# Optimization experiments

Measured on AMD Instinct MI355X. Metric: run time of the kernel, lower is better.

Reference implementation:

```python
import jax, jax.numpy as jnp
import numpy as np

S, B, V, E, H = 64, 32, 32000, 512, 1024


def gru_cell(x, h, Wih, Whh, bih, bhh):
    # PyTorch GRU cell math. x: [B, in], h: [B, H]
    gi = x @ Wih.T + bih          # [B, 3H]
    gh = h @ Whh.T + bhh          # [B, 3H]
    ir, iz, inn = jnp.split(gi, 3, axis=-1)
    hr, hz, hn = jnp.split(gh, 3, axis=-1)
    r = jax.nn.sigmoid(ir + hr)
    z = jax.nn.sigmoid(iz + hz)
    n = jnp.tanh(inn + r * hn)
    return (1.0 - z) * n + z * h


def run_gru(xs, h0, Wih, Whh, bih, bhh):
    def step(h, x):
        h = gru_cell(x, h, Wih, Whh, bih, bhh)
        return h, h
    _, hs = jax.lax.scan(step, h0, xs)
    return hs  # [S, B, H]


def setup_inputs():
    key = jax.random.key(0)
    ks = jax.random.split(key, 24)
    n = lambda k, shp, s=0.05: (jax.random.normal(k, shp, jnp.float32) * s)
    inp = {
        "input_seq": jax.random.randint(ks[0], (S, B), 0, V),
        "target_seq": jax.random.randint(ks[1], (S, B), 0, V),
        "emb": n(ks[2], (V, E)),
        # bidirectional encoder GRU (forward / backward directions)
        "enc_Wih_f": n(ks[3], (3 * H, E)), "enc_Whh_f": n(ks[4], (3 * H, H)),
        "enc_bih_f": n(ks[5], (3 * H,)),  "enc_bhh_f": n(ks[6], (3 * H,)),
        "enc_Wih_b": n(ks[7], (3 * H, E)), "enc_Whh_b": n(ks[8], (3 * H, H)),
        "enc_bih_b": n(ks[9], (3 * H,)),  "enc_bhh_b": n(ks[10], (3 * H,)),
        "encoder_init": n(ks[11], (2, H), 0.1),
        # decoder GRU: input = token(E) + glimpse(2H) + last_output(E)
        "dec_Wih": n(ks[12], (3 * H, 2 * E + 2 * H)), "dec_Whh": n(ks[13], (3 * H, H)),
        "dec_bih": n(ks[14], (3 * H,)), "dec_bhh": n(ks[15], (3 * H,)),
        "dec_init_h": n(ks[16], (H,), 0.1),
        "dec_init_out": n(ks[17], (E,), 0.1),
        "attn_W1": n(ks[18], (H, 3 * H)),  # Linear(3H -> H, bias=False)
        "attn_W2": n(ks[19], (1, H)),      # Linear(H -> 1, bias=False)
        "out_W": n(ks[20], (V, H)), "out_b": n(ks[21], (V,)),
    }
    return inp


def reference(input_seq, target_seq, emb,
              enc_Wih_f, enc_Whh_f, enc_bih_f, enc_bhh_f,
              enc_Wih_b, enc_Whh_b, enc_bih_b, enc_bhh_b, encoder_init,
              dec_Wih, dec_Whh, dec_bih, dec_bhh, dec_init_h, dec_init_out,
              attn_W1, attn_W2, out_W, out_b):
    x = emb[input_seq]            # [S, B, E]
    tgt = emb[target_seq]         # [S, B, E]
    bsz = x.shape[1]

    # bidirectional encoder
    h0f = jnp.broadcast_to(encoder_init[0], (bsz, H))
    h0b = jnp.broadcast_to(encoder_init[1], (bsz, H))
    fwd = run_gru(x, h0f, enc_Wih_f, enc_Whh_f, enc_bih_f, enc_bhh_f)
    bwd = run_gru(x[::-1], h0b, enc_Wih_b, enc_Whh_b, enc_bih_b, enc_bhh_b)[::-1]
    enc = jnp.concatenate([fwd, bwd], axis=-1)  # [S, B, 2H]

    def step(carry, inp_t):
        h, last_out = carry                      # [B,H], [B,E]
        tok, tg = inp_t                          # [B,E], [B,E]
        hexp = jnp.broadcast_to(h[None], (S, bsz, H))
        a = jnp.concatenate([enc, hexp], axis=-1)            # [S, B, 3H]
        scores = jnp.tanh(a @ attn_W1.T) @ attn_W2.T          # [S, B, 1]
        # NOTE: original uses nn.Softmax(dim=1) on [S,B,1] -> softmax over BATCH dim
        w = jax.nn.softmax(scores, axis=1)
        glimpse = (enc * w).sum(axis=0)                       # [B, 2H]
        dec_in = jnp.concatenate([tok, glimpse, last_out], axis=-1)
        h = gru_cell(dec_in, h, dec_Wih, dec_Whh, dec_bih, dec_bhh)
        probs = jax.nn.softmax(h @ out_W.T + out_b, axis=1)   # [B, V]
        return (h, tg), probs

    h0 = jnp.broadcast_to(dec_init_h, (bsz, H))
    o0 = jnp.broadcast_to(dec_init_out, (bsz, E))
    _, outs = jax.lax.scan(step, (h0, o0), (x, tgt))
    return outs  # [S, B, V]
```

## Files before the change

### kernel.cpp

```cpp
#include <hip/hip_runtime.h>
#include <hip/hip_bf16.h>

#define S_ 64
#define B_ 32
#define V_ 32000
#define E_ 512
#define H_ 1024
#define H3_ 3072

typedef __hip_bfloat16 bf16;
typedef __attribute__((ext_vector_type(8))) short s8v;
typedef __attribute__((ext_vector_type(4))) float f4;
typedef unsigned long long ull;

__device__ __forceinline__ float b2f(bf16 x){ return __bfloat162float(x); }
__device__ __forceinline__ bf16  f2b(float x){ return __float2bfloat16(x); }
__device__ __forceinline__ float bfu2f(unsigned short u){
  union { unsigned u; float f; } c; c.u = ((unsigned)u) << 16; return c.f;
}
#define MFMA16(a,b,c) __builtin_amdgcn_mfma_f32_16x16x32_bf16((a),(b),(c),0,0,0)

__device__ __forceinline__ float fsigmoid(float x){ return 1.f/(1.f + __expf(-x)); }
__device__ __forceinline__ float ftanh(float x){ float e2 = __expf(2.f*x); return 1.f - 2.f/(e2 + 1.f); }

__global__ __launch_bounds__(256) void cast_bf16_k(const float* __restrict__ s, bf16* __restrict__ d, int n8){
  int stride = gridDim.x*256;
  for (int i = blockIdx.x*256 + threadIdx.x; i < n8; i += stride){
    f4 a = *((const f4*)s + (size_t)i*2);
    f4 b = *((const f4*)s + (size_t)i*2 + 1);
    union { s8v v; bf16 h[8]; } o;
    #pragma unroll
    for (int k=0;k<4;k++){ o.h[k]=f2b(a[k]); o.h[4+k]=f2b(b[k]); }
    *((s8v*)d + i) = o.v;
  }
}
__global__ __launch_bounds__(256) void gather_x_k(const float* __restrict__ emb, const int* __restrict__ seq, bf16* __restrict__ d){
  int i = blockIdx.x*256 + threadIdx.x;
  int row = i >> 6, e8 = i & 63;
  const float* src = emb + (size_t)seq[row]*E_;
  f4 a = *((const f4*)src + e8*2);
  f4 b = *((const f4*)src + e8*2 + 1);
  union { s8v v; bf16 h[8]; } o;
  #pragma unroll
  for (int k=0;k<4;k++){ o.h[k]=f2b(a[k]); o.h[4+k]=f2b(b[k]); }
  *((s8v*)d + i) = o.v;
}
__global__ __launch_bounds__(256) void gather_lo_k(const float* __restrict__ emb, const int* __restrict__ tseq, const float* __restrict__ o0, bf16* __restrict__ d){
  int i = blockIdx.x*256 + threadIdx.x;
  int row = i >> 6, e8 = i & 63;
  int t = row >> 5, b = row & 31;
  const float* src = (t == 0) ? o0 : (emb + (size_t)tseq[(t-1)*B_ + b]*E_);
  f4 a = *((const f4*)src + e8*2);
  f4 c = *((const f4*)src + e8*2 + 1);
  union { s8v v; bf16 h[8]; } o;
  #pragma unroll
  for (int k=0;k<4;k++){ o.h[k]=f2b(a[k]); o.h[4+k]=f2b(c[k]); }
  *((s8v*)d + i) = o.v;
}

template<int WB16, int ACC>
__global__ __launch_bounds__(256) void gemm_bt(const bf16* __restrict__ A, int lda,
                                               const bf16* __restrict__ B, int ldb,
                                               const float* __restrict__ bias,
                                               void* __restrict__ Cp, int ldc, int K)
{
  __shared__ bf16 a_sm[128][40];
  __shared__ bf16 b_sm[128][40];
  const int tid = threadIdx.x;
  const int m0 = blockIdx.y*128, n0 = blockIdx.x*128;
  const int w = tid>>6, l = tid&63;
  const int wm = w>>1, wn = w&1;
  f4 acc[4][4];
  #pragma unroll
  for (int i=0;i<4;i++)
    #pragma unroll
    for (int j=0;j<4;j++) acc[i][j] = (f4){0.f,0.f,0.f,0.f};
  const int srow = tid>>1, skc = (tid&1)*16;
  const int ar = l&15, koff = (l>>4)*8;
  for (int k0 = 0; k0 < K; k0 += 32){
    __syncthreads();
    const s8v* pa = (const s8v*)(A + (size_t)(m0+srow)*lda + k0 + skc);
    const s8v* pb = (const s8v*)(B + (size_t)(n0+srow)*ldb + k0 + skc);
    *(s8v*)&a_sm[srow][skc]   = pa[0];
    *(s8v*)&a_sm[srow][skc+8] = pa[1];
    *(s8v*)&b_sm[srow][skc]   = pb[0];
    *(s8v*)&b_sm[srow][skc+8] = pb[1];
    __syncthreads();
    s8v av[4], bv[4];
    #pragma unroll
    for (int i=0;i<4;i++) av[i] = *(const s8v*)&a_sm[wm*64 + i*16 + ar][koff];
    #pragma unroll
    for (int j=0;j<4;j++) bv[j] = *(const s8v*)&b_sm[wn*64 + j*16 + ar][koff];
    #pragma unroll
    for (int i=0;i<4;i++)
      #pragma unroll
      for (int j=0;j<4;j++)
        acc[i][j] = MFMA16(av[i], bv[j], acc[i][j]);
  }
  const int rb = (l>>4)*4;
  #pragma unroll
  for (int i=0;i<4;i++){
    #pragma unroll
    for (int j=0;j<4;j++){
      int col = n0 + wn*64 + j*16 + ar;
      float badd = bias ? bias[col] : 0.f;
      #pragma unroll
      for (int r=0;r<4;r++){
        int row = m0 + wm*64 + i*16 + rb + r;
        size_t idx = (size_t)row*ldc + col;
        float v = acc[i][j][r] + badd;
        if (ACC) v += ((const float*)Cp)[idx];
        if (WB16) ((bf16*)Cp)[idx] = f2b(v);
        else      ((float*)Cp)[idx] = v;
      }
    }
  }
}

__global__ __launch_bounds__(256) void enc_init_k(const float* __restrict__ enc_init,
                                                  bf16* __restrict__ hb0, float* __restrict__ hfE){
  int i = blockIdx.x*256 + threadIdx.x;
  int base = i*8;
  int dir = base>>15, rem = base&32767, col = rem&1023;
  const float* sp = enc_init + dir*H_ + col;
  f4 a = *(const f4*)sp, b = *(const f4*)(sp+4);
  union { s8v v; bf16 h[8]; } o;
  #pragma unroll
  for (int k=0;k<4;k++){ o.h[k]=f2b(a[k]); o.h[4+k]=f2b(b[k]); }
  *(s8v*)(hb0 + dir*32768 + rem) = o.v;
  *(f4*)(hfE + dir*32768 + rem) = a;
  *(f4*)(hfE + dir*32768 + rem + 4) = b;
}
__global__ __launch_bounds__(256) void dec_init_k(const float* __restrict__ dinh,
                                                  bf16* __restrict__ hd0, float* __restrict__ hfD){
  int i = blockIdx.x*256 + threadIdx.x;
  int base = i*8;
  int col = base&1023;
  const float* sp = dinh + col;
  f4 a = *(const f4*)sp, b = *(const f4*)(sp+4);
  union { s8v v; bf16 h[8]; } o;
  #pragma unroll
  for (int k=0;k<4;k++){ o.h[k]=f2b(a[k]); o.h[4+k]=f2b(b[k]); }
  *(s8v*)(hd0 + base) = o.v;
  *(f4*)(hfD + base) = a;
  *(f4*)(hfD + base + 4) = b;
}

__global__ __launch_bounds__(256) void enc_step_k(
  const float* __restrict__ gi_f, const float* __restrict__ gi_b,
  const bf16* __restrict__ whhf, const bf16* __restrict__ whhb,
  const float* __restrict__ bhhf, const float* __restrict__ bhhb,
  const bf16* __restrict__ hrd_base,
  bf16* __restrict__ hwr_base,
  float* __restrict__ hfE,
  bf16* __restrict__ enc_out, int s)
{
  __shared__ bf16 hst[16][1032];
  __shared__ bf16 hsT[16][64];
  const int tid = threadIdx.x, bid = blockIdx.x;
  const int w = tid>>6, l = tid&63;
  const int lr = l&15, koff = (l>>4)*8, rb = (l>>4)*4;
  const int x = bid&7, g3 = bid>>3;
  const int dir = x>>2;
  const int mt = g3>>2;
  const int jtb = (x&3)*16 + (g3&3)*4;
  const int jt = jtb + w;
  const int col = jt*16 + lr;
  const bf16* W    = dir ? whhb : whhf;
  const float* gi  = dir ? gi_b : gi_f;
  const float* bhh = dir ? bhhb : bhhf;
  const float br_ = bhh[col], bz_ = bhh[H_+col], bn_ = bhh[2*H_+col];
  const bf16* pr = W + (size_t)(jt*16 + lr)*H_ + koff;
  const bf16* pz = pr + (size_t)H_*H_;
  const bf16* pn = pz + (size_t)H_*H_;
  {
    const bf16* src = hrd_base + dir*32768 + (size_t)mt*16*H_;
    #pragma unroll
    for (int c = 0; c < 8; ++c){
      int g = c*256 + tid;
      int row = g>>7, off = g&127;
      *(s8v*)&hst[row][off*8] = *(const s8v*)(src + (size_t)row*H_ + off*8);
    }
  }
  __syncthreads();
  f4 accr = (f4){0,0,0,0}, accz = (f4){0,0,0,0}, accn = (f4){0,0,0,0};
  #pragma unroll 4
  for (int k0 = 0; k0 < H_; k0 += 32){
    s8v a = *(const s8v*)&hst[lr][koff + k0];
    accr = MFMA16(a, *(const s8v*)(pr + k0), accr);
    accz = MFMA16(a, *(const s8v*)(pz + k0), accz);
    accn = MFMA16(a, *(const s8v*)(pn + k0), accn);
  }
  const int es = dir ? (63 - s) : s;
  #pragma unroll
  for (int ri = 0; ri < 4; ++ri){
    const int b_ = mt*16 + rb + ri;
    const size_t gr = (size_t)(es*B_ + b_)*H3_;
    float ir = gi[gr + col], iz = gi[gr + H_ + col], inn = gi[gr + 2*H_ + col];
    float rg = fsigmoid(ir + accr[ri] + br_);
    float zg = fsigmoid(iz + accz[ri] + bz_);
    float ng = ftanh(inn + rg*(accn[ri] + bn_));
    float hold = hfE[dir*32768 + b_*H_ + col];
    float hnew = (1.f - zg)*ng + zg*hold;
    hfE[dir*32768 + b_*H_ + col] = hnew;
    hsT[rb+ri][w*16+lr] = f2b(hnew);
  }
  __syncthreads();
  {
    const int row = tid>>4, seg = tid&15;
    ull v = *(ull*)&hsT[row][seg*4];
    *(ull*)(hwr_base + dir*32768 + (size_t)(mt*16+row)*H_ + jtb*16 + seg*4) = v;
    *(ull*)(enc_out + (size_t)(es*B_ + mt*16+row)*2048 + dir*H_ + jtb*16 + seg*4) = v;
  }
}

__global__ __launch_bounds__(256) void dec_k1(
  const bf16* __restrict__ hd,
  const bf16* __restrict__ whhd, const float* __restrict__ bhhd,
  const bf16* __restrict__ w1b,
  float* __restrict__ gh, bf16* __restrict__ hW1b)
{
  __shared__ bf16 hst[16][1032];
  __shared__ float ghT[16][128];
  __shared__ bf16 hwT[16][128];
  const int tid = threadIdx.x, bid = blockIdx.x;
  const int w = tid>>6, l = tid&63;
  const int lr = l&15, koff = (l>>4)*8;
  const bool isP = bid < 16;
  const int hmt = isP ? (bid&1) : ((bid-16)&1);
  {
    const bf16* src = hd + (size_t)hmt*16*H_;
    #pragma unroll
    for (int c = 0; c < 8; ++c){
      int g = c*256 + tid;
      int row = g>>7, off = g&127;
      *(s8v*)&hst[row][off*8] = *(const s8v*)(src + (size_t)row*H_ + off*8);
    }
  }
  __syncthreads();
  if (isP){
    const int x2 = bid>>1;
    const int pjt0 = x2*8 + w*2;
    #pragma unroll
    for (int q = 0; q < 2; ++q){
      const bf16* pb = w1b + (size_t)((pjt0+q)*16 + lr)*H3_ + 2048 + koff;
      f4 acc = (f4){0,0,0,0};
      #pragma unroll 4
      for (int k0 = 0; k0 < H_; k0 += 32)
        acc = MFMA16(*(const s8v*)&hst[lr][koff+k0], *(const s8v*)(pb+k0), acc);
      #pragma unroll
      for (int r = 0; r < 4; ++r)
        hwT[(l>>4)*4+r][(w*2+q)*16 + lr] = f2b(acc[r]);
    }
    __syncthreads();
    #pragma unroll
    for (int i = 0; i < 2; ++i){
      int idx = tid + i*256;
      int row = idx>>5, seg = idx&31;
      *(ull*)(hW1b + (size_t)(hmt*16+row)*H_ + x2*128 + seg*4) = *(ull*)&hwT[row][seg*4];
    }
  } else {
    const int gb = bid - 16;
    const int rest = gb>>1;
    const int x3 = rest/3, gkk = rest%3;
    const int ntb = x3*24 + gkk*8;
    #pragma unroll
    for (int q = 0; q < 2; ++q){
      const int nt = ntb + w*2 + q;
      const bf16* pb = whhd + (size_t)(nt*16 + lr)*H_ + koff;
      const float bv = bhhd[nt*16 + lr];
      f4 acc = (f4){0,0,0,0};
      #pragma unroll 4
      for (int k0 = 0; k0 < H_; k0 += 32)
        acc = MFMA16(*(const s8v*)&hst[lr][koff+k0], *(const s8v*)(pb+k0), acc);
      #pragma unroll
      for (int r = 0; r < 4; ++r)
        ghT[(l>>4)*4+r][(w*2+q)*16 + lr] = acc[r] + bv;
    }
    __syncthreads();
    #pragma unroll
    for (int i = 0; i < 4; ++i){
      int idx = tid + i*256;
      int row = idx>>6, seg = idx&63;
      union{ float f[2]; ull u; } pk;
      pk.f[0] = ghT[row][seg*2]; pk.f[1] = ghT[row][seg*2+1];
      *(ull*)(gh + (size_t)(hmt*16+row)*H3_ + ntb*16 + seg*2) = pk.u;
    }
  }
}

__global__ __launch_bounds__(256) void dec_k2(
  const bf16* __restrict__ encW1b, const bf16* __restrict__ hW1b,
  const float* __restrict__ attnW2, float* __restrict__ wat)
{
  __shared__ float w2st[1024];
  __shared__ float scl[32];
  const int tid = threadIdx.x, s = blockIdx.x;
  w2st[tid] = attnW2[tid];
  w2st[tid+256] = attnW2[tid+256];
  w2st[tid+512] = attnW2[tid+512];
  w2st[tid+768] = attnW2[tid+768];
  __syncthreads();
  const int b = tid>>3, part = tid&7;
  const bf16* hp = hW1b + (size_t)b*H_ + part*128;
  const bf16* ep = encW1b + ((size_t)s*B_ + b)*H_ + part*128;
  const float* wp = w2st + part*128;
  float p = 0.f;
  #pragma unroll 4
  for (int ii = 0; ii < 16; ++ii){
    union { s8v v; unsigned short uu[8]; } hv, ev;
    hv.v = *(const s8v*)(hp + ii*8);
    ev.v = *(const s8v*)(ep + ii*8);
    #pragma unroll
    for (int k = 0; k < 8; ++k){
      float xx = bfu2f(ev.uu[k]) + bfu2f(hv.uu[k]);
      p += wp[ii*8+k]*ftanh(xx);
    }
  }
  p += __shfl_xor(p,1); p += __shfl_xor(p,2); p += __shfl_xor(p,4);
  if (part == 0) scl[b] = p;
  __syncthreads();
  if (tid < 32){
    float v = scl[tid];
    float m = v;
    #pragma unroll
    for (int o = 1; o <= 16; o <<= 1) m = fmaxf(m, __shfl_xor(m, o));
    float e = __expf(v - m);
    float Z = e;
    #pragma unroll
    for (int o = 1; o <= 16; o <<= 1) Z += __shfl_xor(Z, o);
    wat[s*B_ + tid] = e/Z;
  }
}

__global__ __launch_bounds__(256) void dec_k3(
  const float* __restrict__ gi_t,
  const bf16* __restrict__ encWgb, const float* __restrict__ gh,
  const float* __restrict__ wat,
  float* __restrict__ hfD, bf16* __restrict__ hd_w, bf16* __restrict__ hall_t)
{
  __shared__ float watst[64];
  __shared__ float part_[4][3][256];
  __shared__ bf16 hnewst[256];
  const int tid = threadIdx.x, bid = blockIdx.x;
  const int x = bid&7, g3 = bid>>3;
  const int db = 4*x + (g3&3), jq = g3>>2;
  const int jD = jq*256 + tid;
  if (tid < 64) watst[tid] = wat[tid*B_ + db];
  __syncthreads();
  const int lane = tid&63, wv = tid>>6;
  const int j0 = jq*256 + lane*4;
  f4 g0 = (f4){0,0,0,0}, g1 = (f4){0,0,0,0}, g2 = (f4){0,0,0,0};
  #pragma unroll 4
  for (int i = 0; i < 16; ++i){
    const int s2 = wv*16 + i;
    const float wt = watst[s2];
    const bf16* ro = encWgb + ((size_t)s2*B_ + db)*H3_;
    union{ ull u; unsigned short us[4]; } v0, v1, v2;
    v0.u = *(const ull*)(ro + j0);
    v1.u = *(const ull*)(ro + H_ + j0);
    v2.u = *(const ull*)(ro + 2*H_ + j0);
    #pragma unroll
    for (int k = 0; k < 4; ++k){
      g0[k] += wt*bfu2f(v0.us[k]);
      g1[k] += wt*bfu2f(v1.us[k]);
      g2[k] += wt*bfu2f(v2.us[k]);
    }
  }
  *(f4*)&part_[wv][0][lane*4] = g0;
  *(f4*)&part_[wv][1][lane*4] = g1;
  *(f4*)&part_[wv][2][lane*4] = g2;
  __syncthreads();
  float G0 = part_[0][0][tid]+part_[1][0][tid]+part_[2][0][tid]+part_[3][0][tid];
  float G1 = part_[0][1][tid]+part_[1][1][tid]+part_[2][1][tid]+part_[3][1][tid];
  float G2 = part_[0][2][tid]+part_[1][2][tid]+part_[2][2][tid]+part_[3][2][tid];
  const float* gp = gi_t + (size_t)db*H3_ + jD;
  float ir  = gp[0]    + G0;
  float iz  = gp[H_]   + G1;
  float inn = gp[2*H_] + G2;
  float hr_ = gh[(size_t)db*H3_ + jD];
  float hz_ = gh[(size_t)db*H3_ + H_ + jD];
  float hn_ = gh[(size_t)db*H3_ + 2*H_ + jD];
  float rg = fsigmoid(ir + hr_);
  float zg = fsigmoid(iz + hz_);
  float ng = ftanh(inn + rg*hn_);
  float hold = hfD[(size_t)db*H_ + jD];
  float hnew = (1.f - zg)*ng + zg*hold;
  hfD[(size_t)db*H_ + jD] = hnew;
  hnewst[tid] = f2b(hnew);
  __syncthreads();
  if (tid < 64){
    ull v = *(ull*)&hnewst[tid*4];
    *(ull*)(hd_w + (size_t)db*H_ + jq*256 + tid*4) = v;
    *(ull*)(hall_t + (size_t)db*H_ + jq*256 + tid*4) = v;
  }
}

__global__ __launch_bounds__(256) void softmax_rows_k(float* __restrict__ out){
  __shared__ float wm[4], wl[4];
  const int tid = threadIdx.x;
  float* p = out + (size_t)blockIdx.x*V_;
  float m = -1e30f, lsum = 0.f;
  for (int j = tid; j < V_; j += 256){
    float v = p[j];
    float mn = fmaxf(m, v);
    lsum = lsum*__expf(m - mn) + __expf(v - mn);
    m = mn;
  }
  #pragma unroll
  for (int o = 32; o; o >>= 1){
    float mo = __shfl_xor(m, o), lo_ = __shfl_xor(lsum, o);
    float mn = fmaxf(m, mo);
    lsum = lsum*__expf(m - mn) + lo_*__expf(mo - mn);
    m = mn;
  }
  if ((tid&63)==0){ wm[tid>>6] = m; wl[tid>>6] = lsum; }
  __syncthreads();
  float M = fmaxf(fmaxf(wm[0],wm[1]), fmaxf(wm[2],wm[3]));
  float L = wl[0]*__expf(wm[0]-M) + wl[1]*__expf(wm[1]-M)
          + wl[2]*__expf(wm[2]-M) + wl[3]*__expf(wm[3]-M);
  float inv = 1.f/L;
  for (int j = tid; j < V_; j += 256) p[j] = __expf(p[j]-M)*inv;
}

extern "C" void kernel_launch(void* const* d_in, const int* in_sizes, int n_in,
                              void* d_out, int out_size, void* d_ws, size_t ws_size,
                              hipStream_t stream)
{
  (void)in_sizes; (void)n_in; (void)out_size; (void)ws_size;
  const int*   iseq  = (const int*)d_in[0];
  const int*   tseq  = (const int*)d_in[1];
  const float* emb   = (const float*)d_in[2];
  const float* wihf  = (const float*)d_in[3];
  const float* whhf_f= (const float*)d_in[4];
  const float* bihf  = (const float*)d_in[5];
  const float* bhhf  = (const float*)d_in[6];
  const float* wihb  = (const float*)d_in[7];
  const float* whhb_f= (const float*)d_in[8];
  const float* bihb  = (const float*)d_in[9];
  const float* bhhb  = (const float*)d_in[10];
  const float* einit = (const float*)d_in[11];
  const float* wihd  = (const float*)d_in[12];
  const float* whhd_f= (const float*)d_in[13];
  const float* bihd  = (const float*)d_in[14];
  const float* bhhd  = (const float*)d_in[15];
  const float* dinh  = (const float*)d_in[16];
  const float* dino  = (const float*)d_in[17];
  const float* w1    = (const float*)d_in[18];
  const float* w2    = (const float*)d_in[19];
  const float* outw  = (const float*)d_in[20];
  const float* outb  = (const float*)d_in[21];
  float* out = (float*)d_out;

  char* ws = (char*)d_ws;
  size_t off = 0;
  auto alloc = [&](size_t bytes)->char*{ char* p = ws + off; off += (bytes + 255) & ~(size_t)255; return p; };
  bf16* x_b      = (bf16*)alloc((size_t)2048*512*2);
  bf16* lo_b     = (bf16*)alloc((size_t)2048*512*2);
  bf16* wihf_b   = (bf16*)alloc((size_t)3072*512*2);
  bf16* wihb_b   = (bf16*)alloc((size_t)3072*512*2);
  bf16* whhf_b   = (bf16*)alloc((size_t)3072*1024*2);
  bf16* whhb_b   = (bf16*)alloc((size_t)3072*1024*2);
  bf16* wihd_b   = (bf16*)alloc((size_t)3072*3072*2);
  bf16* whhd_b   = (bf16*)alloc((size_t)3072*1024*2);
  bf16* w1_b     = (bf16*)alloc((size_t)1024*3072*2);
  bf16* outw_b   = (bf16*)alloc((size_t)32000*1024*2);
  float* gi_f    = (float*)alloc((size_t)2048*3072*4);
  float* gi_b    = (float*)alloc((size_t)2048*3072*4);
  float* gi_d    = (float*)alloc((size_t)2048*3072*4);
  bf16* enc_b    = (bf16*)alloc((size_t)2048*2048*2);
  bf16* encW1_b  = (bf16*)alloc((size_t)2048*1024*2);
  bf16* encWg_b  = (bf16*)alloc((size_t)2048*3072*2);
  bf16*  henc_b  = (bf16*)alloc((size_t)2*65536*2);
  float* hfE     = (float*)alloc((size_t)2*32768*4);
  bf16*  hdb     = (bf16*)alloc((size_t)2*32768*2);
  float* hfD     = (float*)alloc((size_t)32768*4);
  bf16*  hW1b    = (bf16*)alloc((size_t)32768*2);
  float* ghb     = (float*)alloc((size_t)32*3072*4);
  float* wat     = (float*)alloc((size_t)64*32*4);
  bf16*  hall_b  = (bf16*)alloc((size_t)2048*1024*2);

  auto cgrid = [](int n8){ int g = (n8 + 255)/256; return g > 2048 ? 2048 : g; };
  gather_x_k <<<512, 256, 0, stream>>>(emb, iseq, x_b);
  gather_lo_k<<<512, 256, 0, stream>>>(emb, tseq, dino, lo_b);
  cast_bf16_k<<<cgrid(196608),  256, 0, stream>>>(wihf,   wihf_b, 196608);
  cast_bf16_k<<<cgrid(196608),  256, 0, stream>>>(wihb,   wihb_b, 196608);
  cast_bf16_k<<<cgrid(393216),  256, 0, stream>>>(whhf_f, whhf_b, 393216);
  cast_bf16_k<<<cgrid(393216),  256, 0, stream>>>(whhb_f, whhb_b, 393216);
  cast_bf16_k<<<cgrid(1179648), 256, 0, stream>>>(wihd,   wihd_b, 1179648);
  cast_bf16_k<<<cgrid(393216),  256, 0, stream>>>(whhd_f, whhd_b, 393216);
  cast_bf16_k<<<cgrid(393216),  256, 0, stream>>>(w1,     w1_b,   393216);
  cast_bf16_k<<<cgrid(4096000), 256, 0, stream>>>(outw,   outw_b, 4096000);

  gemm_bt<0,0><<<dim3(24,16), 256, 0, stream>>>(x_b, 512, wihf_b,      512,  bihf,    gi_f, 3072, 512);
  gemm_bt<0,0><<<dim3(24,16), 256, 0, stream>>>(x_b, 512, wihb_b,      512,  bihb,    gi_b, 3072, 512);
  gemm_bt<0,0><<<dim3(24,16), 256, 0, stream>>>(x_b, 512, wihd_b,      3072, bihd,    gi_d, 3072, 512);
  gemm_bt<0,1><<<dim3(24,16), 256, 0, stream>>>(lo_b,512, wihd_b+2560, 3072, nullptr, gi_d, 3072, 512);

  enc_init_k<<<32, 256, 0, stream>>>(einit, henc_b, hfE);
  for (int s = 0; s < 64; ++s){
    const bf16* hrd = henc_b + (size_t)(s&1)*65536;
    bf16*       hwr = henc_b + (size_t)((s+1)&1)*65536;
    enc_step_k<<<64, 256, 0, stream>>>(gi_f, gi_b, whhf_b, whhb_b, bhhf, bhhb,
                                       hrd, hwr, hfE, enc_b, s);
  }

  gemm_bt<1,0><<<dim3(8,16),  256, 0, stream>>>(enc_b, 2048, w1_b,       3072, nullptr, encW1_b, 1024, 2048);
  gemm_bt<1,0><<<dim3(24,16), 256, 0, stream>>>(enc_b, 2048, wihd_b+512, 3072, nullptr, encWg_b, 3072, 2048);

  dec_init_k<<<16, 256, 0, stream>>>(dinh, hdb, hfD);
  for (int t = 0; t < 64; ++t){
    const bf16* hdr = hdb + (size_t)(t&1)*32768;
    bf16*       hdw = hdb + (size_t)((t+1)&1)*32768;
    dec_k1<<<64, 256, 0, stream>>>(hdr, whhd_b, bhhd, w1_b, ghb, hW1b);
    dec_k2<<<64, 256, 0, stream>>>(encW1_b, hW1b, w2, wat);
    dec_k3<<<128, 256, 0, stream>>>(gi_d + (size_t)t*B_*H3_, encWg_b, ghb, wat,
                                    hfD, hdw, hall_b + (size_t)t*B_*H_);
  }

  gemm_bt<0,0><<<dim3(250,16), 256, 0, stream>>>(hall_b, 1024, outw_b, 1024, outb, out, 32000, 1024);
  softmax_rows_k<<<2048, 256, 0, stream>>>(out);
}
```

Before: 3.279 ms.

## Fuse decoder attention score kernel into hidden-projection kernel and batch weight casts

Merges the decoder per-step kernels from three to two. The h·W1 projection and the tanh/W2 attention-score reduction now run in the same blocks of the first kernel, each writing partial scores per quarter of H, and the batch softmax moves into the gate kernel. It also combines the forward and backward encoder input GEMMs into a single 6144-wide GEMM with a concatenated bias, and groups the weight casts into fewer launches. The goal is fewer launches and less serialisation in the 64-step decoder loop. The cost is redundant softmax work in every gate block and an extra partial-score buffer.

```diff
diff --git a/kernel.cpp b/kernel.cpp
--- a/kernel.cpp
+++ b/kernel.cpp
@@ -24,6 +24,36 @@
 __device__ __forceinline__ float ftanh(float x){ float e2 = __expf(2.f*x); return 1.f - 2.f/(e2 + 1.f); }
 
 __global__ __launch_bounds__(256) void cast_bf16_k(const float* __restrict__ s, bf16* __restrict__ d, int n8){
+  int stride = gridDim.x*256;
+  for (int i = blockIdx.x*256 + threadIdx.x; i < n8; i += stride){
+    f4 a = *((const f4*)s + (size_t)i*2);
+    f4 b = *((const f4*)s + (size_t)i*2 + 1);
+    union { s8v v; bf16 h[8]; } o;
+    #pragma unroll
+    for (int k=0;k<4;k++){ o.h[k]=f2b(a[k]); o.h[4+k]=f2b(b[k]); }
+    *((s8v*)d + i) = o.v;
+  }
+}
+__global__ __launch_bounds__(256) void cast2_k(const float* __restrict__ s0, const float* __restrict__ s1,
+                                               bf16* __restrict__ d0, bf16* __restrict__ d1, int n8){
+  const float* s = blockIdx.y ? s1 : s0;
+  bf16* d = blockIdx.y ? d1 : d0;
+  int stride = gridDim.x*256;
+  for (int i = blockIdx.x*256 + threadIdx.x; i < n8; i += stride){
+    f4 a = *((const f4*)s + (size_t)i*2);
+    f4 b = *((const f4*)s + (size_t)i*2 + 1);
+    union { s8v v; bf16 h[8]; } o;
+    #pragma unroll
+    for (int k=0;k<4;k++){ o.h[k]=f2b(a[k]); o.h[4+k]=f2b(b[k]); }
+    *((s8v*)d + i) = o.v;
+  }
+}
+__global__ __launch_bounds__(256) void cast4_k(const float* __restrict__ s0, const float* __restrict__ s1,
+                                               const float* __restrict__ s2, const float* __restrict__ s3,
+                                               bf16* __restrict__ d0, bf16* __restrict__ d1,
+                                               bf16* __restrict__ d2, bf16* __restrict__ d3, int n8){
+  const float* s = (blockIdx.y==0)?s0:(blockIdx.y==1)?s1:(blockIdx.y==2)?s2:s3;
+  bf16* d = (blockIdx.y==0)?d0:(blockIdx.y==1)?d1:(blockIdx.y==2)?d2:d3;
   int stride = gridDim.x*256;
   for (int i = blockIdx.x*256 + threadIdx.x; i < n8; i += stride){
     f4 a = *((const f4*)s + (size_t)i*2);
@@ -118,7 +148,9 @@
 }
 
 __global__ __launch_bounds__(256) void enc_init_k(const float* __restrict__ enc_init,
-                                                  bf16* __restrict__ hb0, float* __restrict__ hfE){
+                                                  const float* __restrict__ bihf, const float* __restrict__ bihb,
+                                                  bf16* __restrict__ hb0, float* __restrict__ hfE,
+                                                  float* __restrict__ bias_fb){
   int i = blockIdx.x*256 + threadIdx.x;
   int base = i*8;
   int dir = base>>15, rem = base&32767, col = rem&1023;
@@ -130,6 +162,7 @@
   *(s8v*)(hb0 + dir*32768 + rem) = o.v;
   *(f4*)(hfE + dir*32768 + rem) = a;
   *(f4*)(hfE + dir*32768 + rem + 4) = b;
+  if (i < 6144) bias_fb[i] = (i < 3072) ? bihf[i] : bihb[i-3072];
 }
 __global__ __launch_bounds__(256) void dec_init_k(const float* __restrict__ dinh,
                                                   bf16* __restrict__ hd0, float* __restrict__ hfD){
@@ -147,13 +180,11 @@
 }
 
 __global__ __launch_bounds__(256) void enc_step_k(
-  const float* __restrict__ gi_f, const float* __restrict__ gi_b,
+  const float* __restrict__ gi_fb,
   const bf16* __restrict__ whhf, const bf16* __restrict__ whhb,
   const float* __restrict__ bhhf, const float* __restrict__ bhhb,
-  const bf16* __restrict__ hrd_base,
-  bf16* __restrict__ hwr_base,
-  float* __restrict__ hfE,
-  bf16* __restrict__ enc_out, int s)
+  const bf16* __restrict__ hrd_base, bf16* __restrict__ hwr_base,
+  float* __restrict__ hfE, bf16* __restrict__ enc_out, int s)
 {
   __shared__ bf16 hst[16][1032];
   __shared__ bf16 hsT[16][64];
@@ -167,7 +198,6 @@
   const int jt = jtb + w;
   const int col = jt*16 + lr;
   const bf16* W    = dir ? whhb : whhf;
-  const float* gi  = dir ? gi_b : gi_f;
   const float* bhh = dir ? bhhb : bhhf;
   const float br_ = bhh[col], bz_ = bhh[H_+col], bn_ = bhh[2*H_+col];
   const bf16* pr = W + (size_t)(jt*16 + lr)*H_ + koff;
@@ -192,11 +222,12 @@
     accn = MFMA16(a, *(const s8v*)(pn + k0), accn);
   }
   const int es = dir ? (63 - s) : s;
+  const int dcol = dir*3072 + col;
   #pragma unroll
   for (int ri = 0; ri < 4; ++ri){
     const int b_ = mt*16 + rb + ri;
-    const size_t gr = (size_t)(es*B_ + b_)*H3_;
-    float ir = gi[gr + col], iz = gi[gr + H_ + col], inn = gi[gr + 2*H_ + col];
+    const size_t gr = (size_t)(es*B_ + b_)*6144;
+    float ir = gi_fb[gr + dcol], iz = gi_fb[gr + 1024 + dcol], inn = gi_fb[gr + 2048 + dcol];
     float rg = fsigmoid(ir + accr[ri] + br_);
     float zg = fsigmoid(iz + accz[ri] + bz_);
     float ng = ftanh(inn + rg*(accn[ri] + bn_));
@@ -214,56 +245,37 @@
   }
 }
 
-__global__ __launch_bounds__(256) void dec_k1(
+__global__ __launch_bounds__(256) void dec_kA(
   const bf16* __restrict__ hd,
   const bf16* __restrict__ whhd, const float* __restrict__ bhhd,
   const bf16* __restrict__ w1b,
-  float* __restrict__ gh, bf16* __restrict__ hW1b)
+  const bf16* __restrict__ encW1b,
+  const float* __restrict__ attnW2,
+  float* __restrict__ gh,
+  float* __restrict__ sc4)
 {
   __shared__ bf16 hst[16][1032];
   __shared__ float ghT[16][128];
-  __shared__ bf16 hwT[16][128];
+  __shared__ bf16 hbst[1024];
+  __shared__ float hw1s[256];
   const int tid = threadIdx.x, bid = blockIdx.x;
   const int w = tid>>6, l = tid&63;
   const int lr = l&15, koff = (l>>4)*8;
-  const bool isP = bid < 16;
-  const int hmt = isP ? (bid&1) : ((bid-16)&1);
-  {
-    const bf16* src = hd + (size_t)hmt*16*H_;
-    #pragma unroll
-    for (int c = 0; c < 8; ++c){
-      int g = c*256 + tid;
-      int row = g>>7, off = g&127;
-      *(s8v*)&hst[row][off*8] = *(const s8v*)(src + (size_t)row*H_ + off*8);
-    }
-  }
-  __syncthreads();
-  if (isP){
-    const int x2 = bid>>1;
-    const int pjt0 = x2*8 + w*2;
-    #pragma unroll
-    for (int q = 0; q < 2; ++q){
-      const bf16* pb = w1b + (size_t)((pjt0+q)*16 + lr)*H3_ + 2048 + koff;
-      f4 acc = (f4){0,0,0,0};
-      #pragma unroll 4
-      for (int k0 = 0; k0 < H_; k0 += 32)
-        acc = MFMA16(*(const s8v*)&hst[lr][koff+k0], *(const s8v*)(pb+k0), acc);
-      #pragma unroll
-      for (int r = 0; r < 4; ++r)
-        hwT[(l>>4)*4+r][(w*2+q)*16 + lr] = f2b(acc[r]);
-    }
-    __syncthreads();
-    #pragma unroll
-    for (int i = 0; i < 2; ++i){
-      int idx = tid + i*256;
-      int row = idx>>5, seg = idx&31;
-      *(ull*)(hW1b + (size_t)(hmt*16+row)*H_ + x2*128 + seg*4) = *(ull*)&hwT[row][seg*4];
-    }
-  } else {
-    const int gb = bid - 16;
-    const int rest = gb>>1;
+  if (bid < 48){
+    const int gmt = bid&1;
+    const int rest = bid>>1;
     const int x3 = rest/3, gkk = rest%3;
     const int ntb = x3*24 + gkk*8;
+    {
+      const bf16* src = hd + (size_t)gmt*16*H_;
+      #pragma unroll
+      for (int c = 0; c < 8; ++c){
+        int g = c*256 + tid;
+        int row = g>>7, off = g&127;
+        *(s8v*)&hst[row][off*8] = *(const s8v*)(src + (size_t)row*H_ + off*8);
+      }
+    }
+    __syncthreads();
     #pragma unroll
     for (int q = 0; q < 2; ++q){
       const int nt = ntb + w*2 + q;
@@ -284,59 +296,59 @@
       int row = idx>>6, seg = idx&63;
       union{ float f[2]; ull u; } pk;
       pk.f[0] = ghT[row][seg*2]; pk.f[1] = ghT[row][seg*2+1];
-      *(ull*)(gh + (size_t)(hmt*16+row)*H3_ + ntb*16 + seg*2) = pk.u;
-    }
-  }
-}
-
-__global__ __launch_bounds__(256) void dec_k2(
-  const bf16* __restrict__ encW1b, const bf16* __restrict__ hW1b,
-  const float* __restrict__ attnW2, float* __restrict__ wat)
-{
-  __shared__ float w2st[1024];
-  __shared__ float scl[32];
-  const int tid = threadIdx.x, s = blockIdx.x;
-  w2st[tid] = attnW2[tid];
-  w2st[tid+256] = attnW2[tid+256];
-  w2st[tid+512] = attnW2[tid+512];
-  w2st[tid+768] = attnW2[tid+768];
-  __syncthreads();
-  const int b = tid>>3, part = tid&7;
-  const bf16* hp = hW1b + (size_t)b*H_ + part*128;
-  const bf16* ep = encW1b + ((size_t)s*B_ + b)*H_ + part*128;
-  const float* wp = w2st + part*128;
-  float p = 0.f;
-  #pragma unroll 4
-  for (int ii = 0; ii < 16; ++ii){
-    union { s8v v; unsigned short uu[8]; } hv, ev;
-    hv.v = *(const s8v*)(hp + ii*8);
-    ev.v = *(const s8v*)(ep + ii*8);
-    #pragma unroll
-    for (int k = 0; k < 8; ++k){
-      float xx = bfu2f(ev.uu[k]) + bfu2f(hv.uu[k]);
-      p += wp[ii*8+k]*ftanh(xx);
-    }
-  }
-  p += __shfl_xor(p,1); p += __shfl_xor(p,2); p += __shfl_xor(p,4);
-  if (part == 0) scl[b] = p;
-  __syncthreads();
-  if (tid < 32){
-    float v = scl[tid];
-    float m = v;
-    #pragma unroll
-    for (int o = 1; o <= 16; o <<= 1) m = fmaxf(m, __shfl_xor(m, o));
-    float e = __expf(v - m);
-    float Z = e;
-    #pragma unroll
-    for (int o = 1; o <= 16; o <<= 1) Z += __shfl_xor(Z, o);
-    wat[s*B_ + tid] = e/Z;
-  }
-}
-
-__global__ __launch_bounds__(256) void dec_k3(
+      *(ull*)(gh + (size_t)(gmt*16+row)*H3_ + ntb*16 + seg*2) = pk.u;
+    }
+  } else {
+    const int idx = bid - 48;
+    const int b = idx>>2, q = idx&3;
+    if (tid < 128) *(s8v*)&hbst[tid*8] = *(const s8v*)(hd + (size_t)b*H_ + tid*8);
+    __syncthreads();
+    const bf16* pb0 = w1b + (size_t)(q*256 + (w*4+0)*16 + lr)*H3_ + 2048 + koff;
+    const bf16* pb1 = w1b + (size_t)(q*256 + (w*4+1)*16 + lr)*H3_ + 2048 + koff;
+    const bf16* pb2 = w1b + (size_t)(q*256 + (w*4+2)*16 + lr)*H3_ + 2048 + koff;
+    const bf16* pb3 = w1b + (size_t)(q*256 + (w*4+3)*16 + lr)*H3_ + 2048 + koff;
+    f4 a0 = (f4){0,0,0,0}, a1 = (f4){0,0,0,0}, a2 = (f4){0,0,0,0}, a3 = (f4){0,0,0,0};
+    #pragma unroll 4
+    for (int k0 = 0; k0 < H_; k0 += 32){
+      s8v a = *(const s8v*)&hbst[koff + k0];
+      a0 = MFMA16(a, *(const s8v*)(pb0 + k0), a0);
+      a1 = MFMA16(a, *(const s8v*)(pb1 + k0), a1);
+      a2 = MFMA16(a, *(const s8v*)(pb2 + k0), a2);
+      a3 = MFMA16(a, *(const s8v*)(pb3 + k0), a3);
+    }
+    if (l < 16){
+      hw1s[(w*4+0)*16 + l] = a0[0];
+      hw1s[(w*4+1)*16 + l] = a1[0];
+      hw1s[(w*4+2)*16 + l] = a2[0];
+      hw1s[(w*4+3)*16 + l] = a3[0];
+    }
+    __syncthreads();
+    const int s = tid>>2, part = tid&3;
+    const bf16* ep = encW1b + ((size_t)s*B_ + b)*H_ + q*256 + part*64;
+    const float* w2p = attnW2 + q*256 + part*64;
+    const float* hp = hw1s + part*64;
+    float p = 0.f;
+    #pragma unroll 2
+    for (int ii = 0; ii < 8; ++ii){
+      union { s8v v; unsigned short uu[8]; } ev;
+      ev.v = *(const s8v*)(ep + ii*8);
+      f4 wa = *(const f4*)(w2p + ii*8);
+      f4 wb = *(const f4*)(w2p + ii*8 + 4);
+      #pragma unroll
+      for (int k = 0; k < 8; ++k){
+        float xx = bfu2f(ev.uu[k]) + hp[ii*8+k];
+        p += (k<4 ? wa[k] : wb[k-4])*ftanh(xx);
+      }
+    }
+    p += __shfl_xor(p,1); p += __shfl_xor(p,2);
+    if (part == 0) sc4[q*2048 + s*32 + b] = p;
+  }
+}
+
+__global__ __launch_bounds__(256) void dec_kB(
   const float* __restrict__ gi_t,
   const bf16* __restrict__ encWgb, const float* __restrict__ gh,
-  const float* __restrict__ wat,
+  const float* __restrict__ sc4,
   float* __restrict__ hfD, bf16* __restrict__ hd_w, bf16* __restrict__ hall_t)
 {
   __shared__ float watst[64];
@@ -346,7 +358,27 @@
   const int x = bid&7, g3 = bid>>3;
   const int db = 4*x + (g3&3), jq = g3>>2;
   const int jD = jq*256 + tid;
-  if (tid < 64) watst[tid] = wat[tid*B_ + db];
+  if (tid < 64){
+    const int s = tid;
+    f4 v[8];
+    #pragma unroll
+    for (int c = 0; c < 8; ++c) v[c] = *(const f4*)(sc4 + s*32 + c*4);
+    #pragma unroll
+    for (int q = 1; q < 4; ++q)
+      #pragma unroll
+      for (int c = 0; c < 8; ++c) v[c] += *(const f4*)(sc4 + q*2048 + s*32 + c*4);
+    float m = -1e30f;
+    #pragma unroll
+    for (int c = 0; c < 8; ++c)
+      #pragma unroll
+      for (int k = 0; k < 4; ++k) m = fmaxf(m, v[c][k]);
+    float Z = 0.f;
+    #pragma unroll
+    for (int c = 0; c < 8; ++c)
+      #pragma unroll
+      for (int k = 0; k < 4; ++k) Z += __expf(v[c][k] - m);
+    watst[s] = __expf(v[db>>2][db&3] - m)/Z;
+  }
   __syncthreads();
   const int lane = tid&63, wv = tid>>6;
   const int j0 = jq*256 + lane*4;
@@ -465,9 +497,9 @@
   bf16* whhd_b   = (bf16*)alloc((size_t)3072*1024*2);
   bf16* w1_b     = (bf16*)alloc((size_t)1024*3072*2);
   bf16* outw_b   = (bf16*)alloc((size_t)32000*1024*2);
-  float* gi_f    = (float*)alloc((size_t)2048*3072*4);
-  float* gi_b    = (float*)alloc((size_t)2048*3072*4);
+  float* gi_fb   = (float*)alloc((size_t)2048*6144*4);
   float* gi_d    = (float*)alloc((size_t)2048*3072*4);
+  float* bias_fb = (float*)alloc((size_t)6144*4);
   bf16* enc_b    = (bf16*)alloc((size_t)2048*2048*2);
   bf16* encW1_b  = (bf16*)alloc((size_t)2048*1024*2);
   bf16* encWg_b  = (bf16*)alloc((size_t)2048*3072*2);
@@ -475,33 +507,27 @@
   float* hfE     = (float*)alloc((size_t)2*32768*4);
   bf16*  hdb     = (bf16*)alloc((size_t)2*32768*2);
   float* hfD     = (float*)alloc((size_t)32768*4);
-  bf16*  hW1b    = (bf16*)alloc((size_t)32768*2);
   float* ghb     = (float*)alloc((size_t)32*3072*4);
-  float* wat     = (float*)alloc((size_t)64*32*4);
+  float* sc4     = (float*)alloc((size_t)4*64*32*4);
   bf16*  hall_b  = (bf16*)alloc((size_t)2048*1024*2);
 
-  auto cgrid = [](int n8){ int g = (n8 + 255)/256; return g > 2048 ? 2048 : g; };
   gather_x_k <<<512, 256, 0, stream>>>(emb, iseq, x_b);
   gather_lo_k<<<512, 256, 0, stream>>>(emb, tseq, dino, lo_b);
-  cast_bf16_k<<<cgrid(196608),  256, 0, stream>>>(wihf,   wihf_b, 196608);
-  cast_bf16_k<<<cgrid(196608),  256, 0, stream>>>(wihb,   wihb_b, 196608);
-  cast_bf16_k<<<cgrid(393216),  256, 0, stream>>>(whhf_f, whhf_b, 393216);
-  cast_bf16_k<<<cgrid(393216),  256, 0, stream>>>(whhb_f, whhb_b, 393216);
-  cast_bf16_k<<<cgrid(1179648), 256, 0, stream>>>(wihd,   wihd_b, 1179648);
-  cast_bf16_k<<<cgrid(393216),  256, 0, stream>>>(whhd_f, whhd_b, 393216);
-  cast_bf16_k<<<cgrid(393216),  256, 0, stream>>>(w1,     w1_b,   393216);
-  cast_bf16_k<<<cgrid(4096000), 256, 0, stream>>>(outw,   outw_b, 4096000);
-
-  gemm_bt<0,0><<<dim3(24,16), 256, 0, stream>>>(x_b, 512, wihf_b,      512,  bihf,    gi_f, 3072, 512);
-  gemm_bt<0,0><<<dim3(24,16), 256, 0, stream>>>(x_b, 512, wihb_b,      512,  bihb,    gi_b, 3072, 512);
-  gemm_bt<0,0><<<dim3(24,16), 256, 0, stream>>>(x_b, 512, wihd_b,      3072, bihd,    gi_d, 3072, 512);
-  gemm_bt<0,1><<<dim3(24,16), 256, 0, stream>>>(lo_b,512, wihd_b+2560, 3072, nullptr, gi_d, 3072, 512);
-
-  enc_init_k<<<32, 256, 0, stream>>>(einit, henc_b, hfE);
+  cast2_k<<<dim3(768,2),  256, 0, stream>>>(wihf, wihb, wihf_b, wihb_b, 196608);
+  cast4_k<<<dim3(768,4),  256, 0, stream>>>(whhf_f, whhb_f, whhd_f, w1,
+                                            whhf_b, whhb_b, whhd_b, w1_b, 393216);
+  cast_bf16_k<<<2048, 256, 0, stream>>>(wihd, wihd_b, 1179648);
+  cast_bf16_k<<<2048, 256, 0, stream>>>(outw, outw_b, 4096000);
+  enc_init_k<<<32, 256, 0, stream>>>(einit, bihf, bihb, henc_b, hfE, bias_fb);
+
+  gemm_bt<0,0><<<dim3(48,16), 256, 0, stream>>>(x_b, 512, wihf_b,      512,  bias_fb, gi_fb, 6144, 512);
+  gemm_bt<0,0><<<dim3(24,16), 256, 0, stream>>>(x_b, 512, wihd_b,      3072, bihd,    gi_d,  3072, 512);
+  gemm_bt<0,1><<<dim3(24,16), 256, 0, stream>>>(lo_b,512, wihd_b+2560, 3072, nullptr, gi_d,  3072, 512);
+
   for (int s = 0; s < 64; ++s){
     const bf16* hrd = henc_b + (size_t)(s&1)*65536;
     bf16*       hwr = henc_b + (size_t)((s+1)&1)*65536;
-    enc_step_k<<<64, 256, 0, stream>>>(gi_f, gi_b, whhf_b, whhb_b, bhhf, bhhb,
+    enc_step_k<<<64, 256, 0, stream>>>(gi_fb, whhf_b, whhb_b, bhhf, bhhb,
                                        hrd, hwr, hfE, enc_b, s);
   }
 
@@ -512,9 +538,8 @@
   for (int t = 0; t < 64; ++t){
     const bf16* hdr = hdb + (size_t)(t&1)*32768;
     bf16*       hdw = hdb + (size_t)((t+1)&1)*32768;
-    dec_k1<<<64, 256, 0, stream>>>(hdr, whhd_b, bhhd, w1_b, ghb, hW1b);
-    dec_k2<<<64, 256, 0, stream>>>(encW1_b, hW1b, w2, wat);
-    dec_k3<<<128, 256, 0, stream>>>(gi_d + (size_t)t*B_*H3_, encWg_b, ghb, wat,
+    dec_kA<<<176, 256, 0, stream>>>(hdr, whhd_b, bhhd, w1_b, encW1_b, w2, ghb, sc4);
+    dec_kB<<<128, 256, 0, stream>>>(gi_d + (size_t)t*B_*H3_, encWg_b, ghb, sc4,
                                     hfD, hdw, hall_b + (size_t)t*B_*H_);
   }
 
```

New measurement: 3.483 ms. 6.2% more time.
